# Performance work log

Measured on AMD Instinct MI355X. Metric: run time of the kernel, lower is better.

The kernel has to match this reference:

```python
import jax, jax.numpy as jnp
import numpy as np

B, R, C, OUT, IN = 64, 2048, 32, 32, 16
ROUTING_ITERS = 3


def squash(s, axis=-1):
    s_norm = jnp.linalg.norm(s, axis=axis, keepdims=True)
    scale = s_norm ** 2 / (1.0 + s_norm ** 2)
    return scale * s / (s_norm + 1e-8)


def setup_inputs() -> dict:
    key = jax.random.key(0)
    k1, k2 = jax.random.split(key)
    x = jax.random.normal(k1, (B, R, IN), dtype=jnp.float32)
    W = jax.random.normal(k2, (1, R, C, OUT, IN), dtype=jnp.float32)
    return {"x": x, "W": W}


def reference(x, W):
    # u_hat[b,r,c,o] = sum_i W[r,c,o,i] * x[b,r,i]
    u_hat = jnp.einsum('rcoi,bri->brco', W[0], x)  # [B,R,C,OUT]
    b = jnp.zeros((x.shape[0], R, C), dtype=x.dtype)
    v = None
    for i in range(ROUTING_ITERS):
        c = jax.nn.softmax(b, axis=2)[..., None]       # [B,R,C,1]
        s = jnp.sum(c * u_hat, axis=1)                 # [B,C,OUT]
        v = squash(s)                                  # [B,C,OUT]
        if i < ROUTING_ITERS - 1:
            b = b + jnp.einsum('brco,bco->brc', u_hat, v)
    return v
```

## Files before the change

### kernel.cpp

```cpp
#include <hip/hip_runtime.h>


#define Bn 64
#define Rn 2048
#define Cn 32
#define On 32
#define In 16
#define RCH 16
#define NRC2 (Rn / RCH)
#define NG 4

typedef _Float16 half4v __attribute__((ext_vector_type(4)));
typedef float floatx4 __attribute__((ext_vector_type(4)));

__global__ __launch_bounds__(256)
void wconv(const float* __restrict__ W, _Float16* __restrict__ Wh) {
    const size_t i = ((size_t)blockIdx.x * 256 + threadIdx.x) * 8;
    const float4 a = *(const float4*)(W + i);
    const float4 b = *(const float4*)(W + i + 4);
    union { _Float16 h[8]; uint4 u; } pk;
    pk.h[0] = (_Float16)a.x; pk.h[1] = (_Float16)a.y;
    pk.h[2] = (_Float16)a.z; pk.h[3] = (_Float16)a.w;
    pk.h[4] = (_Float16)b.x; pk.h[5] = (_Float16)b.y;
    pk.h[6] = (_Float16)b.z; pk.h[7] = (_Float16)b.w;
    *(uint4*)(Wh + i) = pk.u;
}

template <int PHASE>
__global__ __launch_bounds__(512, 2)
void upass(const float* __restrict__ x, const _Float16* __restrict__ Wh,
           const float* __restrict__ vroute, float* __restrict__ s_part) {
    const int tid  = threadIdx.x;
    const int w    = tid >> 6;
    const int lane = tid & 63;
    const int q    = lane >> 4;
    const int bl   = lane & 15;

    const int L  = blockIdx.x;
    const int bg = (L >> 3) & 3;
    const int rc = (L & 7) | ((L >> 5) << 3);
    const int b0 = bg * 16;

    __shared__ __attribute__((aligned(16))) _Float16 xs[RCH * 16 * 20];
    __shared__ __attribute__((aligned(16))) float sums[2][16][8];

    floatx4 vr0[4], vr1[4];
    if constexpr (PHASE > 0) {
        const float* vb = vroute + (size_t)(b0 + bl) * 1024 + 4 * q;
#pragma unroll
        for (int t = 0; t < 4; ++t) {
            vr0[t] = *(const floatx4*)(vb + (w * 4 + t) * 32);
            vr1[t] = *(const floatx4*)(vb + (w * 4 + t) * 32 + 16);
        }
    }

#pragma unroll
    for (int k = 0; k < 2; ++k) {
        const int u  = tid + k * 512;
        const int rr = u >> 6, bb = (u >> 2) & 15, iq = u & 3;
        const float4 xv = *(const float4*)(x + (size_t)(b0 + bb) * (Rn * In) +
                                           (size_t)(rc * RCH + rr) * In + iq * 4);
        union { _Float16 h[4]; uint2 u2; } p;
        p.h[0] = (_Float16)xv.x; p.h[1] = (_Float16)xv.y;
        p.h[2] = (_Float16)xv.z; p.h[3] = (_Float16)xv.w;
        *(uint2*)(xs + (rr * 16 + bb) * 20 + iq * 4) = p.u2;
    }
    __syncthreads();

    floatx4 accS[8];
#pragma unroll
    for (int m = 0; m < 8; ++m) accS[m] = (floatx4){0.f, 0.f, 0.f, 0.f};

    const _Float16* Wp = Wh + ((size_t)(rc * RCH) * 1024 + w * 128 + bl) * 16 + 4 * q;

    half4v a[8];
#pragma unroll
    for (int m = 0; m < 8; ++m) a[m] = *(const half4v*)(Wp + m * 256);
    half4v bf = *(const half4v*)(xs + bl * 20 + 4 * q);

    for (int rr = 0; rr < RCH; ++rr) {
        const int rn = (rr + 1 < RCH) ? rr + 1 : rr;
        const _Float16* Wn = Wp + (size_t)rn * 16384;

        if constexpr (PHASE == 0) {
#pragma unroll
            for (int m = 0; m < 8; ++m)
                accS[m] = __builtin_amdgcn_mfma_f32_16x16x16f16(a[m], bf, accS[m], 0, 0, 0);
            const half4v bn = *(const half4v*)(xs + (rn * 16 + bl) * 20 + 4 * q);
#pragma unroll
            for (int m = 0; m < 8; ++m) a[m] = *(const half4v*)(Wn + m * 256);
            bf = bn;
        } else {
            floatx4 D[8];
#pragma unroll
            for (int m = 0; m < 8; ++m)
                D[m] = __builtin_amdgcn_mfma_f32_16x16x16f16(
                           a[m], bf, (floatx4){0.f, 0.f, 0.f, 0.f}, 0, 0, 0);

            const half4v bn = *(const half4v*)(xs + (rn * 16 + bl) * 20 + 4 * q);
#pragma unroll
            for (int m = 0; m < 8; ++m) a[m] = *(const half4v*)(Wn + m * 256);
            bf = bn;

            float e[4], se = 0.f;
#pragma unroll
            for (int t = 0; t < 4; ++t) {
                const floatx4 v0 = vr0[t];
                const floatx4 v1 = vr1[t];
                float lp = D[2*t].x * v0.x + D[2*t].y * v0.y +
                           D[2*t].z * v0.z + D[2*t].w * v0.w +
                           D[2*t+1].x * v1.x + D[2*t+1].y * v1.y +
                           D[2*t+1].z * v1.z + D[2*t+1].w * v1.w;
                lp += __shfl_xor(lp, 16, 64);
                lp += __shfl_xor(lp, 32, 64);
                e[t] = __expf(lp);
                se += e[t];
            }
            if (lane < 16) sums[rr & 1][bl][w] = se;
            asm volatile("s_waitcnt lgkmcnt(0)" ::: "memory");
            __builtin_amdgcn_s_barrier();
            asm volatile("" ::: "memory");
            const floatx4 s0 = *(const floatx4*)(&sums[rr & 1][bl][0]);
            const floatx4 s1 = *(const floatx4*)(&sums[rr & 1][bl][4]);
            const float tot = s0.x + s0.y + s0.z + s0.w +
                              s1.x + s1.y + s1.z + s1.w;
            const float winv = __builtin_amdgcn_rcpf(tot);
#pragma unroll
            for (int t = 0; t < 4; ++t) {
                const float wt = e[t] * winv;
                accS[2*t]   += wt * D[2*t];
                accS[2*t+1] += wt * D[2*t+1];
            }
        }
    }

    const size_t sb = (((size_t)rc * 64 + b0 + bl)) * 1024 + w * 128 + 4 * q;
#pragma unroll
    for (int m = 0; m < 8; ++m)
        *(floatx4*)(s_part + sb + m * 16) = accS[m];
}

__global__ __launch_bounds__(256)
void reduce_squash(const float* __restrict__ sp, float scale,
                   float* __restrict__ vout, const float* __restrict__ vprev,
                   float* __restrict__ vsum) {
    const int b = blockIdx.x >> 3, oct = blockIdx.x & 7;
    const int t = threadIdx.x;
    const int kg = t >> 5, ci = t & 31;
    const size_t base = (size_t)b * 1024 + (size_t)oct * 128 + (size_t)ci * 4;

    floatx4 acc = (floatx4){0.f, 0.f, 0.f, 0.f};
#pragma unroll 4
    for (int k = kg * 16; k < kg * 16 + 16; ++k)
        acc += *(const floatx4*)(sp + (size_t)k * 65536 + base);

    __shared__ __attribute__((aligned(16))) float red[8][128];
    *(floatx4*)(&red[kg][ci * 4]) = acc;
    __syncthreads();

    if (t < 128) {
        float s = 0.f;
#pragma unroll
        for (int g = 0; g < 8; ++g) s += red[g][t];
        s *= scale;
        float n2 = s * s;
        n2 += __shfl_xor(n2, 1, 64);
        n2 += __shfl_xor(n2, 2, 64);
        n2 += __shfl_xor(n2, 4, 64);
        n2 += __shfl_xor(n2, 8, 64);
        n2 += __shfl_xor(n2, 16, 64);
        const float norm = sqrtf(n2);
        const float f = (n2 / (1.f + n2)) / (norm + 1e-8f);
        const float vv = s * f;
        const size_t o = (size_t)b * 1024 + (size_t)oct * 128 + t;
        if (vout) vout[o] = vv;
        if (vsum) vsum[o] = vv + vprev[o];
    }
}

extern "C" void kernel_launch(void* const* d_in, const int* in_sizes, int n_in,
                              void* d_out, int out_size, void* d_ws, size_t ws_size,
                              hipStream_t stream) {
    const float* x = (const float*)d_in[0];
    const float* W = (const float*)d_in[1];
    float* out = (float*)d_out;

    char* ws = (char*)d_ws;
    _Float16* Wh  = (_Float16*)ws;
    float* s_part = (float*)(ws + (size_t)67108864);
    float* v1     = (float*)(ws + (size_t)67108864 + 33554432);
    float* v12    = (float*)(ws + (size_t)67108864 + 33554432 + 262144);

    const int ublocks = NG * NRC2;

    wconv<<<16384, 256, 0, stream>>>(W, Wh);

    upass<0><<<ublocks, 512, 0, stream>>>(x, Wh, nullptr, s_part);
    reduce_squash<<<512, 256, 0, stream>>>(s_part, 1.f / 32.f, v1, nullptr, nullptr);

    upass<1><<<ublocks, 512, 0, stream>>>(x, Wh, v1, s_part);
    reduce_squash<<<512, 256, 0, stream>>>(s_part, 1.f, nullptr, v1, v12);

    upass<2><<<ublocks, 512, 0, stream>>>(x, Wh, v12, s_part);
    reduce_squash<<<512, 256, 0, stream>>>(s_part, 1.f, out, nullptr, nullptr);
}
```

Measured before the change: 311.4 us.

## Process 32 batches per block to reuse W fragments across two MFMA tiles

```diff
diff --git a/kernel.cpp b/kernel.cpp
--- a/kernel.cpp
+++ b/kernel.cpp
@@ -8,7 +8,7 @@
 #define In 16
 #define RCH 16
 #define NRC2 (Rn / RCH)
-#define NG 4
+#define NG 2
 
 typedef _Float16 half4v __attribute__((ext_vector_type(4)));
 typedef float floatx4 __attribute__((ext_vector_type(4)));
@@ -37,46 +37,54 @@
     const int bl   = lane & 15;
 
     const int L  = blockIdx.x;
-    const int bg = (L >> 3) & 3;
-    const int rc = (L & 7) | ((L >> 5) << 3);
-    const int b0 = bg * 16;
-
-    __shared__ __attribute__((aligned(16))) _Float16 xs[RCH * 16 * 20];
-    __shared__ __attribute__((aligned(16))) float sums[2][16][8];
-
-    floatx4 vr0[4], vr1[4];
+    const int bg = (L >> 3) & 1;
+    const int rc = (L & 7) | ((L >> 4) << 3);
+    const int b0 = bg * 32;
+
+    __shared__ __attribute__((aligned(16))) _Float16 xs[RCH * 32 * 20];
+    __shared__ __attribute__((aligned(16))) float sums[2][2][16][8];
+
+    floatx4 v00[4], v01[4], v10[4], v11[4];
     if constexpr (PHASE > 0) {
-        const float* vb = vroute + (size_t)(b0 + bl) * 1024 + 4 * q;
+        const float* vb0 = vroute + (size_t)(b0 + bl) * 1024 + 4 * q;
+        const float* vb1 = vroute + (size_t)(b0 + 16 + bl) * 1024 + 4 * q;
 #pragma unroll
         for (int t = 0; t < 4; ++t) {
-            vr0[t] = *(const floatx4*)(vb + (w * 4 + t) * 32);
-            vr1[t] = *(const floatx4*)(vb + (w * 4 + t) * 32 + 16);
+            const int co = (w * 4 + t) * 32;
+            v00[t] = *(const floatx4*)(vb0 + co);
+            v01[t] = *(const floatx4*)(vb0 + co + 16);
+            v10[t] = *(const floatx4*)(vb1 + co);
+            v11[t] = *(const floatx4*)(vb1 + co + 16);
         }
     }
 
 #pragma unroll
-    for (int k = 0; k < 2; ++k) {
+    for (int k = 0; k < 4; ++k) {
         const int u  = tid + k * 512;
-        const int rr = u >> 6, bb = (u >> 2) & 15, iq = u & 3;
+        const int rr = u >> 7, bb = (u >> 2) & 31, iq = u & 3;
         const float4 xv = *(const float4*)(x + (size_t)(b0 + bb) * (Rn * In) +
                                            (size_t)(rc * RCH + rr) * In + iq * 4);
         union { _Float16 h[4]; uint2 u2; } p;
         p.h[0] = (_Float16)xv.x; p.h[1] = (_Float16)xv.y;
         p.h[2] = (_Float16)xv.z; p.h[3] = (_Float16)xv.w;
-        *(uint2*)(xs + (rr * 16 + bb) * 20 + iq * 4) = p.u2;
+        *(uint2*)(xs + (rr * 32 + bb) * 20 + iq * 4) = p.u2;
     }
     __syncthreads();
 
-    floatx4 accS[8];
-#pragma unroll
-    for (int m = 0; m < 8; ++m) accS[m] = (floatx4){0.f, 0.f, 0.f, 0.f};
+    floatx4 accS0[8], accS1[8];
+#pragma unroll
+    for (int m = 0; m < 8; ++m) {
+        accS0[m] = (floatx4){0.f, 0.f, 0.f, 0.f};
+        accS1[m] = (floatx4){0.f, 0.f, 0.f, 0.f};
+    }
 
     const _Float16* Wp = Wh + ((size_t)(rc * RCH) * 1024 + w * 128 + bl) * 16 + 4 * q;
 
     half4v a[8];
 #pragma unroll
     for (int m = 0; m < 8; ++m) a[m] = *(const half4v*)(Wp + m * 256);
-    half4v bf = *(const half4v*)(xs + bl * 20 + 4 * q);
+    half4v bf0 = *(const half4v*)(xs + bl * 20 + 4 * q);
+    half4v bf1 = *(const half4v*)(xs + (16 + bl) * 20 + 4 * q);
 
     for (int rr = 0; rr < RCH; ++rr) {
         const int rn = (rr + 1 < RCH) ? rr + 1 : rr;
@@ -84,60 +92,81 @@
 
         if constexpr (PHASE == 0) {
 #pragma unroll
-            for (int m = 0; m < 8; ++m)
-                accS[m] = __builtin_amdgcn_mfma_f32_16x16x16f16(a[m], bf, accS[m], 0, 0, 0);
-            const half4v bn = *(const half4v*)(xs + (rn * 16 + bl) * 20 + 4 * q);
+            for (int m = 0; m < 8; ++m) {
+                accS0[m] = __builtin_amdgcn_mfma_f32_16x16x16f16(a[m], bf0, accS0[m], 0, 0, 0);
+                accS1[m] = __builtin_amdgcn_mfma_f32_16x16x16f16(a[m], bf1, accS1[m], 0, 0, 0);
+            }
+            const half4v bn0 = *(const half4v*)(xs + (rn * 32 + bl) * 20 + 4 * q);
+            const half4v bn1 = *(const half4v*)(xs + (rn * 32 + 16 + bl) * 20 + 4 * q);
 #pragma unroll
             for (int m = 0; m < 8; ++m) a[m] = *(const half4v*)(Wn + m * 256);
-            bf = bn;
+            bf0 = bn0; bf1 = bn1;
         } else {
-            floatx4 D[8];
-#pragma unroll
-            for (int m = 0; m < 8; ++m)
-                D[m] = __builtin_amdgcn_mfma_f32_16x16x16f16(
-                           a[m], bf, (floatx4){0.f, 0.f, 0.f, 0.f}, 0, 0, 0);
-
-            const half4v bn = *(const half4v*)(xs + (rn * 16 + bl) * 20 + 4 * q);
+            floatx4 D0[8], D1[8];
+#pragma unroll
+            for (int m = 0; m < 8; ++m) {
+                D0[m] = __builtin_amdgcn_mfma_f32_16x16x16f16(
+                            a[m], bf0, (floatx4){0.f, 0.f, 0.f, 0.f}, 0, 0, 0);
+                D1[m] = __builtin_amdgcn_mfma_f32_16x16x16f16(
+                            a[m], bf1, (floatx4){0.f, 0.f, 0.f, 0.f}, 0, 0, 0);
+            }
+
+            const half4v bn0 = *(const half4v*)(xs + (rn * 32 + bl) * 20 + 4 * q);
+            const half4v bn1 = *(const half4v*)(xs + (rn * 32 + 16 + bl) * 20 + 4 * q);
 #pragma unroll
             for (int m = 0; m < 8; ++m) a[m] = *(const half4v*)(Wn + m * 256);
-            bf = bn;
-
-            float e[4], se = 0.f;
+            bf0 = bn0; bf1 = bn1;
+
+            float e0[4], e1[4], se0 = 0.f, se1 = 0.f;
 #pragma unroll
             for (int t = 0; t < 4; ++t) {
-                const floatx4 v0 = vr0[t];
-                const floatx4 v1 = vr1[t];
-                float lp = D[2*t].x * v0.x + D[2*t].y * v0.y +
-                           D[2*t].z * v0.z + D[2*t].w * v0.w +
-                           D[2*t+1].x * v1.x + D[2*t+1].y * v1.y +
-                           D[2*t+1].z * v1.z + D[2*t+1].w * v1.w;
-                lp += __shfl_xor(lp, 16, 64);
-                lp += __shfl_xor(lp, 32, 64);
-                e[t] = __expf(lp);
-                se += e[t];
-            }
-            if (lane < 16) sums[rr & 1][bl][w] = se;
+                float lp0 = D0[2*t].x * v00[t].x + D0[2*t].y * v00[t].y +
+                            D0[2*t].z * v00[t].z + D0[2*t].w * v00[t].w +
+                            D0[2*t+1].x * v01[t].x + D0[2*t+1].y * v01[t].y +
+                            D0[2*t+1].z * v01[t].z + D0[2*t+1].w * v01[t].w;
+                float lp1 = D1[2*t].x * v10[t].x + D1[2*t].y * v10[t].y +
+                            D1[2*t].z * v10[t].z + D1[2*t].w * v10[t].w +
+                            D1[2*t+1].x * v11[t].x + D1[2*t+1].y * v11[t].y +
+                            D1[2*t+1].z * v11[t].z + D1[2*t+1].w * v11[t].w;
+                lp0 += __shfl_xor(lp0, 16, 64);
+                lp0 += __shfl_xor(lp0, 32, 64);
+                lp1 += __shfl_xor(lp1, 16, 64);
+                lp1 += __shfl_xor(lp1, 32, 64);
+                e0[t] = __expf(lp0); se0 += e0[t];
+                e1[t] = __expf(lp1); se1 += e1[t];
+            }
+            if (lane < 32) sums[rr & 1][q][bl][w] = (q == 0) ? se0 : se1;
             asm volatile("s_waitcnt lgkmcnt(0)" ::: "memory");
             __builtin_amdgcn_s_barrier();
             asm volatile("" ::: "memory");
-            const floatx4 s0 = *(const floatx4*)(&sums[rr & 1][bl][0]);
-            const floatx4 s1 = *(const floatx4*)(&sums[rr & 1][bl][4]);
-            const float tot = s0.x + s0.y + s0.z + s0.w +
-                              s1.x + s1.y + s1.z + s1.w;
-            const float winv = __builtin_amdgcn_rcpf(tot);
+            const floatx4 sa0 = *(const floatx4*)(&sums[rr & 1][0][bl][0]);
+            const floatx4 sa1 = *(const floatx4*)(&sums[rr & 1][0][bl][4]);
+            const floatx4 sb0 = *(const floatx4*)(&sums[rr & 1][1][bl][0]);
+            const floatx4 sb1 = *(const floatx4*)(&sums[rr & 1][1][bl][4]);
+            const float tot0 = sa0.x + sa0.y + sa0.z + sa0.w +
+                               sa1.x + sa1.y + sa1.z + sa1.w;
+            const float tot1 = sb0.x + sb0.y + sb0.z + sb0.w +
+                               sb1.x + sb1.y + sb1.z + sb1.w;
+            const float winv0 = __builtin_amdgcn_rcpf(tot0);
+            const float winv1 = __builtin_amdgcn_rcpf(tot1);
 #pragma unroll
             for (int t = 0; t < 4; ++t) {
-                const float wt = e[t] * winv;
-                accS[2*t]   += wt * D[2*t];
-                accS[2*t+1] += wt * D[2*t+1];
+                const float wt0 = e0[t] * winv0;
+                const float wt1 = e1[t] * winv1;
+                accS0[2*t]   += wt0 * D0[2*t];
+                accS0[2*t+1] += wt0 * D0[2*t+1];
+                accS1[2*t]   += wt1 * D1[2*t];
+                accS1[2*t+1] += wt1 * D1[2*t+1];
             }
         }
     }
 
     const size_t sb = (((size_t)rc * 64 + b0 + bl)) * 1024 + w * 128 + 4 * q;
 #pragma unroll
-    for (int m = 0; m < 8; ++m)
-        *(floatx4*)(s_part + sb + m * 16) = accS[m];
+    for (int m = 0; m < 8; ++m) {
+        *(floatx4*)(s_part + sb + m * 16) = accS0[m];
+        *(floatx4*)(s_part + sb + (size_t)16 * 1024 + m * 16) = accS1[m];
+    }
 }
 
 __global__ __launch_bounds__(256)
@@ -149,10 +178,14 @@
     const int kg = t >> 5, ci = t & 31;
     const size_t base = (size_t)b * 1024 + (size_t)oct * 128 + (size_t)ci * 4;
 
-    floatx4 acc = (floatx4){0.f, 0.f, 0.f, 0.f};
-#pragma unroll 4
-    for (int k = kg * 16; k < kg * 16 + 16; ++k)
-        acc += *(const floatx4*)(sp + (size_t)k * 65536 + base);
+    floatx4 acc0 = (floatx4){0.f, 0.f, 0.f, 0.f};
+    floatx4 acc1 = (floatx4){0.f, 0.f, 0.f, 0.f};
+#pragma unroll
+    for (int k = kg * 16; k < kg * 16 + 16; k += 2) {
+        acc0 += *(const floatx4*)(sp + (size_t)k * 65536 + base);
+        acc1 += *(const floatx4*)(sp + (size_t)(k + 1) * 65536 + base);
+    }
+    const floatx4 acc = acc0 + acc1;
 
     __shared__ __attribute__((aligned(16))) float red[8][128];
     *(floatx4*)(&red[kg][ci * 4]) = acc;
```

Result: faster. 297.5 us (-4.5%).
